# Kernel optimization log

Measured on AMD Instinct MI355X. Metric: run time of the kernel, lower is better.

Reference implementation:

```python
import jax, jax.numpy as jnp
import numpy as np

H, N, D, K = 4, 512, 64, 64  # n_heads, node_num, d_model, sparse_k
TEMP = 0.5
EPS = 1e-10


def setup_inputs() -> dict:
    key = jax.random.key(0)
    k1, k2, k3 = jax.random.split(key, 3)
    feats = jax.random.normal(k1, (H, N, D), jnp.float32)
    # torch Linear init ~ U(-1/sqrt(fan_in), 1/sqrt(fan_in)); Gaussian scale is fine for a baseline
    W_out = jax.random.normal(k2, (2 * D, D), jnp.float32) * (1.0 / np.sqrt(2 * D))
    b_out = jnp.zeros((D,), jnp.float32)
    W_cat = jax.random.normal(k3, (D, 2), jnp.float32) * (1.0 / np.sqrt(D))
    b_cat = jnp.zeros((2,), jnp.float32)
    return {"feats": feats, "W_out": W_out, "b_out": b_out,
            "W_cat": W_cat, "b_cat": b_cat, "sparse_k": K}


def reference(feats, W_out, b_out, W_cat, b_cat, sparse_k):
    H_, N_, D_ = feats.shape
    E = N_ * N_
    e = jnp.arange(E)
    rec_idx = e // N_   # receiver node of edge e (rel_rec one-hot gather)
    snd_idx = e % N_    # sender node of edge e (rel_send one-hot gather)
    # cat([senders, receivers], -1): [H, E, 2D]
    x = jnp.concatenate([feats[:, snd_idx], feats[:, rec_idx]], axis=-1)
    h = jax.nn.relu(x @ W_out + b_out)          # [H, E, D]
    logits = h @ W_cat + b_cat                  # [H, E, 2]
    # gumbel-softmax, hard (straight-through)
    U = jax.random.uniform(jax.random.key(42), logits.shape, jnp.float32)
    g = -jnp.log(-jnp.log(U + EPS) + EPS)
    y_soft = jax.nn.softmax((logits + g) / TEMP, axis=-1)
    y_hard = jax.nn.one_hot(jnp.argmax(y_soft, axis=-1), 2, dtype=y_soft.dtype)
    y = jax.lax.stop_gradient(y_hard - y_soft) + y_soft
    connection_matrix = y[..., 1].reshape(H_, N_, N_)
    connection_prob = jax.nn.softmax(logits, axis=-1)[..., 1]  # [H, E]
    _, top_idx = jax.lax.top_k(connection_prob, sparse_k)      # top-k over edges per head
    sparse_labels = jnp.zeros_like(connection_prob).at[
        jnp.arange(H_)[:, None], top_idx].set(1.0)
    return connection_matrix, connection_prob, sparse_labels
```

## Files before the change

kernel.cpp:

```cpp
#include <hip/hip_runtime.h>
#include <stdint.h>

#define H_ 4
#define N_ 512
#define D_ 64
#define E_ (N_ * N_)
#define HE_ (H_ * E_)
#define EPS_ 1e-10f

__device__ __forceinline__ void tf2x32(unsigned x0, unsigned x1,
                                       unsigned& o0, unsigned& o1) {
  const unsigned ks0 = 0u;
  const unsigned ks1 = 42u;
  const unsigned ks2 = 0x1BD11BDAu ^ ks0 ^ ks1;
  x0 += ks0; x1 += ks1;
#define TFR(r) { x0 += x1; x1 = (x1 << (r)) | (x1 >> (32 - (r))); x1 ^= x0; }
  TFR(13) TFR(15) TFR(26) TFR(6)
  x0 += ks1; x1 += ks2 + 1u;
  TFR(17) TFR(29) TFR(16) TFR(24)
  x0 += ks2; x1 += ks0 + 2u;
  TFR(13) TFR(15) TFR(26) TFR(6)
  x0 += ks0; x1 += ks1 + 3u;
  TFR(17) TFR(29) TFR(16) TFR(24)
  x0 += ks1; x1 += ks2 + 4u;
  TFR(13) TFR(15) TFR(26) TFR(6)
  x0 += ks2; x1 += ks0 + 5u;
#undef TFR
  o0 = x0; o1 = x1;
}

__device__ __forceinline__ unsigned rng_bits(unsigned j) {
  unsigned a, b;
  tf2x32(0u, j, a, b);
  return a ^ b;
}

__device__ __forceinline__ float u01(unsigned bits) {
  return __uint_as_float((bits >> 9) | 0x3f800000u) - 1.0f;
}

__global__ __launch_bounds__(256) void precompute_ab(
    const float* __restrict__ feats, const float* __restrict__ W_out,
    float* __restrict__ A, float* __restrict__ B) {
  int row = blockIdx.x * 4 + (threadIdx.x >> 6);
  int d = threadIdx.x & 63;
  __shared__ float f[4][64];
  f[threadIdx.x >> 6][d] = feats[row * D_ + d];
  __syncthreads();
  const float* fr = f[threadIdx.x >> 6];
  float a = 0.f, b = 0.f;
#pragma unroll 8
  for (int k = 0; k < D_; ++k) {
    float fv = fr[k];
    a = fmaf(fv, W_out[k * D_ + d], a);
    b = fmaf(fv, W_out[(k + D_) * D_ + d], b);
  }
  A[row * D_ + d] = a;
  B[row * D_ + d] = b;
}

__global__ __launch_bounds__(256) void edge_kernel(
    const float* __restrict__ A, const float* __restrict__ B,
    const float* __restrict__ b_out, const float* __restrict__ W_cat,
    const float* __restrict__ b_cat, float* __restrict__ out,
    unsigned long long* __restrict__ blockmax) {
  __shared__ float Ash[128][65];
  __shared__ float Bsh[16][64];
  __shared__ float bsh[64];
  __shared__ float2 wc2[64];
  __shared__ float bc2[2];
  __shared__ unsigned long long wmax[4];

  const int t = threadIdx.x;
  const int h = blockIdx.z;
  const int snd_base = blockIdx.x * 128;
  const int rec_base = blockIdx.y * 16;

  const float4* A4 = (const float4*)(A + (h * N_ + snd_base) * D_);
  for (int i = t; i < 2048; i += 256) {
    float4 v = A4[i];
    int r = i >> 4, c = (i & 15) * 4;
    Ash[r][c] = v.x; Ash[r][c + 1] = v.y; Ash[r][c + 2] = v.z; Ash[r][c + 3] = v.w;
  }
  {
    const float4* B4 = (const float4*)(B + (h * N_ + rec_base) * D_);
    float4 v = B4[t];
    int r = t >> 4, c = (t & 15) * 4;
    *(float4*)&Bsh[r][c] = v;
  }
  if (t < 64) { bsh[t] = b_out[t]; wc2[t] = ((const float2*)W_cat)[t]; }
  if (t == 64) { bc2[0] = b_cat[0]; bc2[1] = b_cat[1]; }
  __syncthreads();

  const int s = t & 63;
  const int rg = (t >> 6) * 4;

  float l0[2][4], l1[2][4];
#pragma unroll
  for (int q = 0; q < 2; ++q)
#pragma unroll
    for (int r = 0; r < 4; ++r) { l0[q][r] = 0.f; l1[q][r] = 0.f; }

#pragma unroll 4
  for (int d = 0; d < 64; ++d) {
    float a0 = Ash[s][d];
    float a1 = Ash[s + 64][d];
    float bd = bsh[d];
    float2 w = wc2[d];
#pragma unroll
    for (int r = 0; r < 4; ++r) {
      float bv = Bsh[rg + r][d];
      float t0 = fmaxf((a0 + bv) + bd, 0.f);
      float t1 = fmaxf((a1 + bv) + bd, 0.f);
      l0[0][r] = fmaf(t0, w.x, l0[0][r]);
      l1[0][r] = fmaf(t0, w.y, l1[0][r]);
      l0[1][r] = fmaf(t1, w.x, l0[1][r]);
      l1[1][r] = fmaf(t1, w.y, l1[1][r]);
    }
  }

  unsigned long long mk = 0ull;
#pragma unroll
  for (int q = 0; q < 2; ++q) {
#pragma unroll
    for (int r = 0; r < 4; ++r) {
      float L0 = l0[q][r] + bc2[0];
      float L1 = l1[q][r] + bc2[1];
      const unsigned snd = (unsigned)(snd_base + s + q * 64);
      const unsigned rec = (unsigned)(rec_base + rg + r);
      const unsigned e = rec * (unsigned)N_ + snd;
      const unsigned base = ((unsigned)h << 18) + e;
      const unsigned j0 = base * 2u;

      float uu0 = u01(rng_bits(j0));
      float uu1 = u01(rng_bits(j0 + 1u));
      float g0 = -logf(-logf(uu0 + EPS_) + EPS_);
      float g1 = -logf(-logf(uu1 + EPS_) + EPS_);

      float A0 = (L0 + g0) / 0.5f;
      float A1 = (L1 + g1) / 0.5f;
      float am = fmaxf(A0, A1);
      float ea0 = expf(A0 - am), ea1 = expf(A1 - am);
      float ss2 = ea0 + ea1;
      float cm = ((ea1 / ss2) > (ea0 / ss2)) ? 1.0f : 0.0f;

      float lm = fmaxf(L0, L1);
      float p0 = expf(L0 - lm), p1 = expf(L1 - lm);
      float pr = p1 / (p0 + p1);

      out[base] = cm;
      out[HE_ + base] = pr;
      out[2 * HE_ + base] = 0.f;

      unsigned long long key =
          ((unsigned long long)__float_as_uint(pr) << 32) | (unsigned)(~e);
      mk = key > mk ? key : mk;
    }
  }

#pragma unroll
  for (int off = 32; off; off >>= 1) {
    unsigned long long o = __shfl_xor(mk, off, 64);
    mk = o > mk ? o : mk;
  }
  if ((t & 63) == 0) wmax[t >> 6] = mk;
  __syncthreads();
  if (t == 0) {
    unsigned long long m = wmax[0];
#pragma unroll
    for (int i = 1; i < 4; ++i) m = wmax[i] > m ? wmax[i] : m;
    blockmax[h * 128 + blockIdx.y * gridDim.x + blockIdx.x] = m;
  }
}

__global__ __launch_bounds__(128) void select_thresh(
    const unsigned long long* __restrict__ blockmax,
    unsigned long long* __restrict__ M64, unsigned* __restrict__ cnt) {
  __shared__ unsigned long long keys[128];
  const int t = threadIdx.x, h = blockIdx.x;
  keys[t] = blockmax[h * 128 + t];
  __syncthreads();
  for (int k = 2; k <= 128; k <<= 1)
    for (int j = k >> 1; j > 0; j >>= 1) {
      int ixj = t ^ j;
      if (ixj > t) {
        unsigned long long a = keys[t], b = keys[ixj];
        bool up = (t & k) == 0;
        if ((a > b) == up) { keys[t] = b; keys[ixj] = a; }
      }
      __syncthreads();
    }
  if (t == 0) { M64[h] = keys[64]; cnt[h] = 0u; }
}

__global__ __launch_bounds__(1024) void compact(
    const float* __restrict__ prob, const unsigned long long* __restrict__ M64,
    unsigned* __restrict__ cnt, unsigned long long* __restrict__ cand) {
  const int h = blockIdx.y;
  const unsigned i4 = (blockIdx.x * 1024u + threadIdx.x) * 4u;
  const unsigned long long thr = M64[h];
  float4 p = *(const float4*)(prob + (unsigned)h * E_ + i4);
  float pv[4] = {p.x, p.y, p.z, p.w};
#pragma unroll
  for (int k = 0; k < 4; ++k) {
    unsigned e = i4 + (unsigned)k;
    unsigned long long key =
        ((unsigned long long)__float_as_uint(pv[k]) << 32) | (unsigned)(~e);
    if (key >= thr) {
      unsigned pos = atomicAdd(&cnt[h], 1u);
      if (pos < 512u) cand[h * 512 + pos] = key;
    }
  }
}

__global__ __launch_bounds__(512) void final_topk(
    const unsigned long long* __restrict__ cand, const unsigned* __restrict__ cnt,
    float* __restrict__ sparse) {
  __shared__ unsigned long long keys[512];
  const int t = threadIdx.x, h = blockIdx.x;
  unsigned n = cnt[h]; if (n > 512u) n = 512u;
  keys[t] = (t < (int)n) ? cand[h * 512 + t] : 0ull;
  __syncthreads();
  for (int k = 2; k <= 512; k <<= 1)
    for (int j = k >> 1; j > 0; j >>= 1) {
      int ixj = t ^ j;
      if (ixj > t) {
        unsigned long long a = keys[t], b = keys[ixj];
        bool up = (t & k) == 0;
        if ((a > b) == up) { keys[t] = b; keys[ixj] = a; }
      }
      __syncthreads();
    }
  if (t >= 448) {
    unsigned e = ~(unsigned)(keys[t] & 0xFFFFFFFFull);
    if (e < (unsigned)E_) sparse[(unsigned)h * E_ + e] = 1.0f;
  }
}

extern "C" void kernel_launch(void* const* d_in, const int* in_sizes, int n_in,
                              void* d_out, int out_size, void* d_ws, size_t ws_size,
                              hipStream_t stream) {
  const float* feats = (const float*)d_in[0];
  const float* W_out = (const float*)d_in[1];
  const float* b_out = (const float*)d_in[2];
  const float* W_cat = (const float*)d_in[3];
  const float* b_cat = (const float*)d_in[4];
  float* out = (float*)d_out;

  float* A = (float*)d_ws;
  float* B = A + H_ * N_ * D_;
  unsigned long long* blockmax = (unsigned long long*)(B + H_ * N_ * D_);
  unsigned long long* M64 = blockmax + H_ * 128;
  unsigned long long* cand = M64 + H_;
  unsigned* cnt = (unsigned*)(cand + H_ * 512);

  precompute_ab<<<dim3(H_ * N_ / 4), dim3(256), 0, stream>>>(feats, W_out, A, B);
  edge_kernel<<<dim3(N_ / 128, N_ / 16, H_), dim3(256), 0, stream>>>(
      A, B, b_out, W_cat, b_cat, out, blockmax);
  select_thresh<<<dim3(H_), dim3(128), 0, stream>>>(blockmax, M64, cnt);
  compact<<<dim3(E_ / 4096, H_), dim3(1024), 0, stream>>>(out + HE_, M64, cnt, cand);
  final_topk<<<dim3(H_), dim3(512), 0, stream>>>(cand, cnt, out + 2 * HE_);
}
```

Baseline: 111.2 us.

## Fuse top-k threshold, compaction and final sort into one kernel; vectorise edge loop

```diff
diff --git a/kernel.cpp b/kernel.cpp
--- a/kernel.cpp
+++ b/kernel.cpp
@@ -41,9 +41,14 @@
 
 __global__ __launch_bounds__(256) void precompute_ab(
     const float* __restrict__ feats, const float* __restrict__ W_out,
-    float* __restrict__ A, float* __restrict__ B) {
+    float* __restrict__ A, float* __restrict__ B,
+    unsigned* __restrict__ cnt, unsigned* __restrict__ done) {
   int row = blockIdx.x * 4 + (threadIdx.x >> 6);
   int d = threadIdx.x & 63;
+  if (blockIdx.x == 0) {
+    if (threadIdx.x < 4) cnt[threadIdx.x] = 0u;
+    else if (threadIdx.x < 8) done[threadIdx.x - 4] = 0u;
+  }
   __shared__ float f[4][64];
   f[threadIdx.x >> 6][d] = feats[row * D_ + d];
   __syncthreads();
@@ -64,10 +69,10 @@
     const float* __restrict__ b_out, const float* __restrict__ W_cat,
     const float* __restrict__ b_cat, float* __restrict__ out,
     unsigned long long* __restrict__ blockmax) {
-  __shared__ float Ash[128][65];
-  __shared__ float Bsh[16][64];
-  __shared__ float bsh[64];
-  __shared__ float2 wc2[64];
+  __shared__ __align__(16) float Ash[128][68];
+  __shared__ __align__(16) float Bsh[16][64];
+  __shared__ float4 bsh4[16];
+  __shared__ float4 wc4[32];
   __shared__ float bc2[2];
   __shared__ unsigned long long wmax[4];
 
@@ -76,20 +81,19 @@
   const int snd_base = blockIdx.x * 128;
   const int rec_base = blockIdx.y * 16;
 
-  const float4* A4 = (const float4*)(A + (h * N_ + snd_base) * D_);
-  for (int i = t; i < 2048; i += 256) {
-    float4 v = A4[i];
-    int r = i >> 4, c = (i & 15) * 4;
-    Ash[r][c] = v.x; Ash[r][c + 1] = v.y; Ash[r][c + 2] = v.z; Ash[r][c + 3] = v.w;
-  }
   {
+    const float4* A4 = (const float4*)(A + (h * N_ + snd_base) * D_);
+    for (int i = t; i < 2048; i += 256) {
+      float4 v = A4[i];
+      *(float4*)&Ash[i >> 4][(i & 15) << 2] = v;
+    }
     const float4* B4 = (const float4*)(B + (h * N_ + rec_base) * D_);
     float4 v = B4[t];
-    int r = t >> 4, c = (t & 15) * 4;
-    *(float4*)&Bsh[r][c] = v;
-  }
-  if (t < 64) { bsh[t] = b_out[t]; wc2[t] = ((const float2*)W_cat)[t]; }
-  if (t == 64) { bc2[0] = b_cat[0]; bc2[1] = b_cat[1]; }
+    *(float4*)&Bsh[t >> 4][(t & 15) << 2] = v;
+  }
+  if (t < 16) bsh4[t] = ((const float4*)b_out)[t];
+  else if (t < 48) wc4[t - 16] = ((const float4*)W_cat)[t - 16];
+  else if (t == 48) { bc2[0] = b_cat[0]; bc2[1] = b_cat[1]; }
   __syncthreads();
 
   const int s = t & 63;
@@ -101,21 +105,33 @@
 #pragma unroll
     for (int r = 0; r < 4; ++r) { l0[q][r] = 0.f; l1[q][r] = 0.f; }
 
-#pragma unroll 4
-  for (int d = 0; d < 64; ++d) {
-    float a0 = Ash[s][d];
-    float a1 = Ash[s + 64][d];
-    float bd = bsh[d];
-    float2 w = wc2[d];
+#pragma unroll
+  for (int d4 = 0; d4 < 16; ++d4) {
+    const float4 a0 = *(const float4*)&Ash[s][d4 << 2];
+    const float4 a1 = *(const float4*)&Ash[s + 64][d4 << 2];
+    const float4 bd = bsh4[d4];
+    const float4 wA = wc4[2 * d4];
+    const float4 wB = wc4[2 * d4 + 1];
 #pragma unroll
     for (int r = 0; r < 4; ++r) {
-      float bv = Bsh[rg + r][d];
-      float t0 = fmaxf((a0 + bv) + bd, 0.f);
-      float t1 = fmaxf((a1 + bv) + bd, 0.f);
-      l0[0][r] = fmaf(t0, w.x, l0[0][r]);
-      l1[0][r] = fmaf(t0, w.y, l1[0][r]);
-      l0[1][r] = fmaf(t1, w.x, l0[1][r]);
-      l1[1][r] = fmaf(t1, w.y, l1[1][r]);
+      const float4 bv = *(const float4*)&Bsh[rg + r][d4 << 2];
+      float t0, t1;
+      t0 = fmaxf((a0.x + bv.x) + bd.x, 0.f);
+      t1 = fmaxf((a1.x + bv.x) + bd.x, 0.f);
+      l0[0][r] = fmaf(t0, wA.x, l0[0][r]); l1[0][r] = fmaf(t0, wA.y, l1[0][r]);
+      l0[1][r] = fmaf(t1, wA.x, l0[1][r]); l1[1][r] = fmaf(t1, wA.y, l1[1][r]);
+      t0 = fmaxf((a0.y + bv.y) + bd.y, 0.f);
+      t1 = fmaxf((a1.y + bv.y) + bd.y, 0.f);
+      l0[0][r] = fmaf(t0, wA.z, l0[0][r]); l1[0][r] = fmaf(t0, wA.w, l1[0][r]);
+      l0[1][r] = fmaf(t1, wA.z, l0[1][r]); l1[1][r] = fmaf(t1, wA.w, l1[1][r]);
+      t0 = fmaxf((a0.z + bv.z) + bd.z, 0.f);
+      t1 = fmaxf((a1.z + bv.z) + bd.z, 0.f);
+      l0[0][r] = fmaf(t0, wB.x, l0[0][r]); l1[0][r] = fmaf(t0, wB.y, l1[0][r]);
+      l0[1][r] = fmaf(t1, wB.x, l0[1][r]); l1[1][r] = fmaf(t1, wB.y, l1[1][r]);
+      t0 = fmaxf((a0.w + bv.w) + bd.w, 0.f);
+      t1 = fmaxf((a1.w + bv.w) + bd.w, 0.f);
+      l0[0][r] = fmaf(t0, wB.z, l0[0][r]); l1[0][r] = fmaf(t0, wB.w, l1[0][r]);
+      l0[1][r] = fmaf(t1, wB.z, l0[1][r]); l1[1][r] = fmaf(t1, wB.w, l1[1][r]);
     }
   }
 
@@ -137,12 +153,7 @@
       float g0 = -logf(-logf(uu0 + EPS_) + EPS_);
       float g1 = -logf(-logf(uu1 + EPS_) + EPS_);
 
-      float A0 = (L0 + g0) / 0.5f;
-      float A1 = (L1 + g1) / 0.5f;
-      float am = fmaxf(A0, A1);
-      float ea0 = expf(A0 - am), ea1 = expf(A1 - am);
-      float ss2 = ea0 + ea1;
-      float cm = ((ea1 / ss2) > (ea0 / ss2)) ? 1.0f : 0.0f;
+      float cm = ((L1 + g1) > (L0 + g0)) ? 1.0f : 0.0f;
 
       float lm = fmaxf(L0, L1);
       float p0 = expf(L0 - lm), p1 = expf(L1 - lm);
@@ -173,67 +184,68 @@
   }
 }
 
-__global__ __launch_bounds__(128) void select_thresh(
-    const unsigned long long* __restrict__ blockmax,
-    unsigned long long* __restrict__ M64, unsigned* __restrict__ cnt) {
-  __shared__ unsigned long long keys[128];
-  const int t = threadIdx.x, h = blockIdx.x;
-  keys[t] = blockmax[h * 128 + t];
-  __syncthreads();
-  for (int k = 2; k <= 128; k <<= 1)
-    for (int j = k >> 1; j > 0; j >>= 1) {
-      int ixj = t ^ j;
-      if (ixj > t) {
-        unsigned long long a = keys[t], b = keys[ixj];
-        bool up = (t & k) == 0;
-        if ((a > b) == up) { keys[t] = b; keys[ixj] = a; }
+__global__ __launch_bounds__(512) void topk_fused(
+    const float* __restrict__ prob, const unsigned long long* __restrict__ blockmax,
+    unsigned* __restrict__ cnt, unsigned* __restrict__ done,
+    unsigned long long* __restrict__ cand, float* __restrict__ sparse) {
+  __shared__ unsigned long long keys[512];
+  __shared__ unsigned long long thrS;
+  __shared__ unsigned tkS;
+  const int t = threadIdx.x, h = blockIdx.y, blk = blockIdx.x;
+
+  if (t < 128) keys[t] = blockmax[h * 128 + t];
+  __syncthreads();
+  if (t < 128) {
+    unsigned long long my = keys[t];
+    int rank = 0;
+    for (int j = 0; j < 128; ++j) rank += (keys[j] > my);
+    if (rank == 63) thrS = my;
+  }
+  __syncthreads();
+  const unsigned long long thr = thrS;
+
+  const unsigned seg = (unsigned)blk * 4096u;
+#pragma unroll
+  for (int i = 0; i < 2; ++i) {
+    const unsigned e0 = seg + (unsigned)i * 2048u + (unsigned)t * 4u;
+    float4 p = *(const float4*)(prob + (unsigned)h * E_ + e0);
+    float pv[4] = {p.x, p.y, p.z, p.w};
+#pragma unroll
+    for (int k2 = 0; k2 < 4; ++k2) {
+      unsigned e = e0 + (unsigned)k2;
+      unsigned long long key =
+          ((unsigned long long)__float_as_uint(pv[k2]) << 32) | (unsigned)(~e);
+      if (key >= thr) {
+        unsigned pos = atomicAdd(&cnt[h], 1u);
+        if (pos < 512u) cand[h * 512 + pos] = key;
       }
-      __syncthreads();
-    }
-  if (t == 0) { M64[h] = keys[64]; cnt[h] = 0u; }
-}
-
-__global__ __launch_bounds__(1024) void compact(
-    const float* __restrict__ prob, const unsigned long long* __restrict__ M64,
-    unsigned* __restrict__ cnt, unsigned long long* __restrict__ cand) {
-  const int h = blockIdx.y;
-  const unsigned i4 = (blockIdx.x * 1024u + threadIdx.x) * 4u;
-  const unsigned long long thr = M64[h];
-  float4 p = *(const float4*)(prob + (unsigned)h * E_ + i4);
-  float pv[4] = {p.x, p.y, p.z, p.w};
-#pragma unroll
-  for (int k = 0; k < 4; ++k) {
-    unsigned e = i4 + (unsigned)k;
-    unsigned long long key =
-        ((unsigned long long)__float_as_uint(pv[k]) << 32) | (unsigned)(~e);
-    if (key >= thr) {
-      unsigned pos = atomicAdd(&cnt[h], 1u);
-      if (pos < 512u) cand[h * 512 + pos] = key;
-    }
-  }
-}
-
-__global__ __launch_bounds__(512) void final_topk(
-    const unsigned long long* __restrict__ cand, const unsigned* __restrict__ cnt,
-    float* __restrict__ sparse) {
-  __shared__ unsigned long long keys[512];
-  const int t = threadIdx.x, h = blockIdx.x;
-  unsigned n = cnt[h]; if (n > 512u) n = 512u;
-  keys[t] = (t < (int)n) ? cand[h * 512 + t] : 0ull;
-  __syncthreads();
-  for (int k = 2; k <= 512; k <<= 1)
-    for (int j = k >> 1; j > 0; j >>= 1) {
-      int ixj = t ^ j;
-      if (ixj > t) {
-        unsigned long long a = keys[t], b = keys[ixj];
-        bool up = (t & k) == 0;
-        if ((a > b) == up) { keys[t] = b; keys[ixj] = a; }
+    }
+  }
+  __syncthreads();
+  if (t == 0) { __threadfence(); tkS = atomicAdd(&done[h], 1u); }
+  __syncthreads();
+
+  if (tkS == 63u) {
+    if (t == 0) __threadfence();
+    __syncthreads();
+    unsigned n = atomicAdd(&cnt[h], 0u);
+    if (n > 512u) n = 512u;
+    keys[t] = (t < (int)n) ? cand[h * 512 + t] : 0ull;
+    __syncthreads();
+    for (int k = 2; k <= 512; k <<= 1)
+      for (int j = k >> 1; j > 0; j >>= 1) {
+        int ixj = t ^ j;
+        if (ixj > t) {
+          unsigned long long a = keys[t], b = keys[ixj];
+          bool up = (t & k) == 0;
+          if ((a > b) == up) { keys[t] = b; keys[ixj] = a; }
+        }
+        __syncthreads();
       }
-      __syncthreads();
-    }
-  if (t >= 448) {
-    unsigned e = ~(unsigned)(keys[t] & 0xFFFFFFFFull);
-    if (e < (unsigned)E_) sparse[(unsigned)h * E_ + e] = 1.0f;
+    if (t >= 448) {
+      unsigned e = ~(unsigned)(keys[t] & 0xFFFFFFFFull);
+      if (e < (unsigned)E_) sparse[(unsigned)h * E_ + e] = 1.0f;
+    }
   }
 }
 
@@ -250,14 +262,14 @@
   float* A = (float*)d_ws;
   float* B = A + H_ * N_ * D_;
   unsigned long long* blockmax = (unsigned long long*)(B + H_ * N_ * D_);
-  unsigned long long* M64 = blockmax + H_ * 128;
-  unsigned long long* cand = M64 + H_;
+  unsigned long long* cand = blockmax + H_ * 128;
   unsigned* cnt = (unsigned*)(cand + H_ * 512);
-
-  precompute_ab<<<dim3(H_ * N_ / 4), dim3(256), 0, stream>>>(feats, W_out, A, B);
+  unsigned* done = cnt + H_;
+
+  precompute_ab<<<dim3(H_ * N_ / 4), dim3(256), 0, stream>>>(feats, W_out, A, B,
+                                                             cnt, done);
   edge_kernel<<<dim3(N_ / 128, N_ / 16, H_), dim3(256), 0, stream>>>(
       A, B, b_out, W_cat, b_cat, out, blockmax);
-  select_thresh<<<dim3(H_), dim3(128), 0, stream>>>(blockmax, M64, cnt);
-  compact<<<dim3(E_ / 4096, H_), dim3(1024), 0, stream>>>(out + HE_, M64, cnt, cand);
-  final_topk<<<dim3(H_), dim3(512), 0, stream>>>(cand, cnt, out + 2 * HE_);
-}
+  topk_fused<<<dim3(64, H_), dim3(512), 0, stream>>>(out + HE_, blockmax, cnt,
+                                                     done, cand, out + 2 * HE_);
+}
```

Result: no change. 110.8 us (-0.3%).
